# Optimization experiments

Measured on AMD Instinct MI355X. Metric: run time of the kernel, lower is better.

## Reference

```python
import jax, jax.numpy as jnp
import numpy as np

EPS = 1e-6
B, T, C = 2, 1024, 2048
H, KV, D = 32, 8, 128
E, F, TOPK = 8, 768, 2


def rmsnorm(x, w):
    xf = x.astype(jnp.float32)
    var = jnp.mean(xf * xf, axis=-1, keepdims=True)
    return w * (xf * jax.lax.rsqrt(var + EPS)).astype(x.dtype)


def rotate_half(x):
    d = x.shape[-1] // 2
    return jnp.concatenate([-x[..., d:], x[..., :d]], axis=-1)


def setup_inputs() -> dict:
    key = jax.random.key(0)
    ks = jax.random.split(key, 12)
    sc = 0.02
    x = jax.random.normal(ks[0], (B, T, C), dtype=jnp.float32)
    # RoPE tables: cos/sin of shape [B, T, D]
    inv_freq = 1.0 / (1e6 ** (np.arange(0, D, 2, dtype=np.float32) / D))
    pos = np.arange(T, dtype=np.float32)
    freqs = pos[:, None] * inv_freq[None, :]          # [T, D/2]
    emb = np.concatenate([freqs, freqs], axis=-1)     # [T, D]
    cos = jnp.broadcast_to(jnp.cos(emb)[None], (B, T, D)).astype(jnp.float32)
    sin = jnp.broadcast_to(jnp.sin(emb)[None], (B, T, D)).astype(jnp.float32)
    return {
        "x": x, "cos": cos, "sin": sin,
        "ln1_w": jnp.ones((C,), jnp.float32),
        "q_w": jax.random.normal(ks[1], (C, H * D), jnp.float32) * sc,
        "k_w": jax.random.normal(ks[2], (C, KV * D), jnp.float32) * sc,
        "v_w": jax.random.normal(ks[3], (C, KV * D), jnp.float32) * sc,
        "o_w": jax.random.normal(ks[4], (H * D, C), jnp.float32) * sc,
        "qn_w": jnp.ones((D,), jnp.float32),
        "kn_w": jnp.ones((D,), jnp.float32),
        "ln2_w": jnp.ones((C,), jnp.float32),
        "gate_w": jax.random.normal(ks[5], (C, E), jnp.float32) * sc,
        "gate_up_w": jax.random.normal(ks[6], (E, C, 2 * F), jnp.float32) * sc,
        "down_w": jax.random.normal(ks[7], (E, F, C), jnp.float32) * sc,
    }


def reference(x, cos, sin, ln1_w, q_w, k_w, v_w, o_w, qn_w, kn_w, ln2_w,
              gate_w, gate_up_w, down_w):
    b, t, c = x.shape
    # ---- attention branch ----
    h = rmsnorm(x, ln1_w)
    q = (h @ q_w).reshape(b, t, H, D)
    k = (h @ k_w).reshape(b, t, KV, D)
    v = (h @ v_w).reshape(b, t, KV, D)
    q = rmsnorm(q, qn_w)
    k = rmsnorm(k, kn_w)
    cb = cos[:, :, None, :]
    sb = sin[:, :, None, :]
    q = q * cb + rotate_half(q) * sb
    k = k * cb + rotate_half(k) * sb
    rep = H // KV
    k = jnp.repeat(k, rep, axis=2)  # [b,t,H,D]
    v = jnp.repeat(v, rep, axis=2)
    scores = jnp.einsum('bthd,bshd->bhts', q, k) / jnp.sqrt(jnp.float32(D))
    causal = jnp.tril(jnp.ones((t, t), dtype=bool))
    scores = jnp.where(causal, scores, jnp.finfo(scores.dtype).min)
    attn = jax.nn.softmax(scores, axis=-1)
    ao = jnp.einsum('bhts,bshd->bthd', attn, v).reshape(b, t, H * D) @ o_w
    x = x + ao
    # ---- MoE branch ----
    h2 = rmsnorm(x, ln2_w)
    hidden = h2.reshape(-1, c)                     # [N, C]
    logits = hidden @ gate_w                       # [N, E]
    rw = jax.nn.softmax(logits.astype(jnp.float32), axis=-1)
    tw, ti = jax.lax.top_k(rw, TOPK)
    tw = tw / (tw.sum(axis=-1, keepdims=True) + 1e-9)
    n = hidden.shape[0]
    routed = jnp.zeros_like(logits).at[jnp.arange(n)[:, None], ti].set(tw.astype(logits.dtype))
    routed = routed / (routed.sum(axis=-1, keepdims=True) + 1e-9)
    gu = jnp.einsum('th,ehq->teq', hidden, gate_up_w)   # [N, E, 2F]
    g, u = jnp.split(gu, 2, axis=-1)
    eo = jnp.einsum('teq,eqh->teh', jax.nn.silu(g) * u, down_w)  # [N, E, C]
    moe = (eo * routed[..., None]).sum(axis=1).reshape(b, t, c)
    return x + moe
```

## Files before the change

kernel.cpp:

```cpp
#include <hip/hip_runtime.h>
#include <hip/hip_bf16.h>

typedef short bf16x8 __attribute__((ext_vector_type(8)));
typedef float f32x4 __attribute__((ext_vector_type(4)));
typedef unsigned short u16;

#define NTOK 2048
#define CDIM 2048
#define TSEQ 1024
#define NH   32
#define NKV  8
#define DH   128
#define NE   8
#define FDIM 768
#define CAP  2048

#define GLOAD_LDS16(g, l) \
  __builtin_amdgcn_global_load_lds((const __attribute__((address_space(1))) void*)(g), \
                                   (__attribute__((address_space(3))) void*)(l), 16, 0, 0)

__device__ __forceinline__ u16 f2bf(float f){
  union { float f; unsigned u; } v; v.f = f;
  unsigned r = v.u + 0x7FFFu + ((v.u >> 16) & 1u);
  return (u16)(r >> 16);
}
__device__ __forceinline__ float bf2f(u16 x){
  union { unsigned u; float f; } v; v.u = ((unsigned)x) << 16; return v.f;
}

__device__ __forceinline__ f32x4 mfma_bf16(bf16x8 a, bf16x8 b, f32x4 c){
  return __builtin_amdgcn_mfma_f32_16x16x32_bf16(a, b, c, 0, 0, 0);
}

__device__ __forceinline__ int xcd_swz(int orig, int nwg){
  int xcd = orig & 7;
  int q = nwg >> 3, r = nwg & 7;
  int base = (xcd < r) ? xcd*(q+1) : r*(q+1) + (xcd-r)*q;
  return base + (orig >> 3);
}

__global__ void cast_transpose(const float* __restrict__ in, u16* __restrict__ out,
                               int R, int Cc, int rstride, int d1,
                               long long s_hi, long long s_lo)
{
  __shared__ float tile[32][33];
  int z = blockIdx.z;
  in += (long long)(z / d1) * s_hi + (long long)(z % d1) * s_lo;
  out += (size_t)z * R * Cc;
  int tx = threadIdx.x & 31, ty = threadIdx.x >> 5;
  int r0 = blockIdx.y * 32, c0 = blockIdx.x * 32;
  #pragma unroll
  for(int i=0;i<4;i++){
    int r = r0 + ty + i*8;
    if(r < R && c0 + tx < Cc) tile[ty + i*8][tx] = in[(size_t)r * rstride + c0 + tx];
  }
  __syncthreads();
  #pragma unroll
  for(int i=0;i<4;i++){
    int c = c0 + ty + i*8;
    if(c < Cc && r0 + tx < R) out[(size_t)c * R + r0 + tx] = f2bf(tile[tx][ty + i*8]);
  }
}

__global__ void transpose_u16(const u16* __restrict__ in, u16* __restrict__ out,
                              int R, int Cc, int rstride, int d1,
                              long long s_hi, long long s_lo)
{
  __shared__ u16 tile[32][34];
  int z = blockIdx.z;
  in += (long long)(z / d1) * s_hi + (long long)(z % d1) * s_lo;
  out += (size_t)z * R * Cc;
  int tx = threadIdx.x & 31, ty = threadIdx.x >> 5;
  int r0 = blockIdx.y * 32, c0 = blockIdx.x * 32;
  #pragma unroll
  for(int i=0;i<4;i++){
    int r = r0 + ty + i*8;
    if(r < R && c0 + tx < Cc) tile[ty + i*8][tx] = in[(size_t)r * rstride + c0 + tx];
  }
  __syncthreads();
  #pragma unroll
  for(int i=0;i<4;i++){
    int c = c0 + ty + i*8;
    if(c < Cc && r0 + tx < R) out[(size_t)c * R + r0 + tx] = tile[tx][ty + i*8];
  }
}

__global__ void rmsnorm_kernel(const float* __restrict__ x, const float* __restrict__ w,
                               u16* __restrict__ outb, float* __restrict__ outf)
{
  __shared__ float sbuf[4];
  int row = blockIdx.x;
  const float* xr = x + (size_t)row * CDIM;
  int t0 = threadIdx.x * 8;
  float4 v0 = *(const float4*)(xr + t0);
  float4 v1 = *(const float4*)(xr + t0 + 4);
  float a[8] = {v0.x,v0.y,v0.z,v0.w,v1.x,v1.y,v1.z,v1.w};
  float ss = 0.f;
  #pragma unroll
  for(int i=0;i<8;i++) ss += a[i]*a[i];
  #pragma unroll
  for(int o=32;o>0;o>>=1) ss += __shfl_xor(ss, o);
  if((threadIdx.x & 63) == 0) sbuf[threadIdx.x >> 6] = ss;
  __syncthreads();
  float tot = sbuf[0]+sbuf[1]+sbuf[2]+sbuf[3];
  float r = rsqrtf(tot * (1.0f/CDIM) + 1e-6f);
  float4 w0 = *(const float4*)(w + t0);
  float4 w1 = *(const float4*)(w + t0 + 4);
  float wv[8] = {w0.x,w0.y,w0.z,w0.w,w1.x,w1.y,w1.z,w1.w};
  #pragma unroll
  for(int i=0;i<8;i++){
    float o = a[i] * r * wv[i];
    outb[(size_t)row*CDIM + t0 + i] = f2bf(o);
    if(outf) outf[(size_t)row*CDIM + t0 + i] = o;
  }
}

__global__ __launch_bounds__(512, 2) void gemm256(const u16* __restrict__ A,
                                                  const u16* __restrict__ Bt,
                                                  u16* __restrict__ Cb,
                                                  int M, int N, int K)
{
  extern __shared__ u16 lds[];
  const int NT = K >> 6;
  int tid = threadIdx.x;
  int lane = tid & 63, g = lane >> 4, cl = lane & 15;
  int wid = tid >> 6, wr = wid >> 2, wc = wid & 3;
  int br = blockIdx.y * 256, bc = blockIdx.x * 256;
  int rowl[4], slotl[4], srcoff[4];
  #pragma unroll
  for(int l=0;l<4;l++){
    int c = l*512 + tid;
    rowl[l]  = c >> 3;
    slotl[l] = c & 7;
    srcoff[l] = (slotl[l] ^ (rowl[l] & 7)) * 8;
  }
  f32x4 acc[8][4];
  #pragma unroll
  for(int m=0;m<8;m++)
    #pragma unroll
    for(int n=0;n<4;n++) acc[m][n] = (f32x4){0.f,0.f,0.f,0.f};

  auto stage = [&](int t, int b){
    int k0 = t << 6;
    #pragma unroll
    for(int l=0;l<4;l++)
      GLOAD_LDS16(A  + (size_t)(br + rowl[l])*K + k0 + srcoff[l],
                  &lds[b*16384 + rowl[l]*64 + slotl[l]*8]);
    #pragma unroll
    for(int l=0;l<4;l++)
      GLOAD_LDS16(Bt + (size_t)(bc + rowl[l])*K + k0 + srcoff[l],
                  &lds[32768 + b*16384 + rowl[l]*64 + slotl[l]*8]);
  };

  stage(0, 0);
  for(int t=0;t<NT;t++){
    int buf = t & 1;
    if(t+1 < NT){
      stage(t+1, buf^1);
      asm volatile("s_waitcnt vmcnt(8)" ::: "memory");
    } else {
      asm volatile("s_waitcnt vmcnt(0)" ::: "memory");
    }
    asm volatile("s_barrier" ::: "memory");
    const u16* As_ = &lds[buf*16384];
    const u16* Bs_ = &lds[32768 + buf*16384];
    __builtin_amdgcn_s_setprio(1);
    #pragma unroll
    for(int kk=0;kk<2;kk++){
      bf16x8 a[8], b[4];
      #pragma unroll
      for(int m=0;m<8;m++){
        int row = wr*128 + m*16 + cl;
        int sl  = ((4*kk + g) ^ (row & 7)) * 8;
        a[m] = *(const bf16x8*)&As_[row*64 + sl];
      }
      #pragma unroll
      for(int n=0;n<4;n++){
        int row = wc*64 + n*16 + cl;
        int sl  = ((4*kk + g) ^ (row & 7)) * 8;
        b[n] = *(const bf16x8*)&Bs_[row*64 + sl];
      }
      #pragma unroll
      for(int m=0;m<8;m++)
        #pragma unroll
        for(int n=0;n<4;n++)
          acc[m][n] = mfma_bf16(a[m], b[n], acc[m][n]);
    }
    __builtin_amdgcn_s_setprio(0);
    asm volatile("s_barrier" ::: "memory");
  }
  #pragma unroll
  for(int m=0;m<8;m++)
    #pragma unroll
    for(int n=0;n<4;n++)
      #pragma unroll
      for(int j=0;j<4;j++){
        int row = br + wr*128 + m*16 + g*4 + j;
        int col = bc + wc*64 + n*16 + cl;
        Cb[(size_t)row*N + col] = f2bf(acc[m][n][j]);
      }
}

__global__ __launch_bounds__(256) void gemm_oproj_pipe(const u16* __restrict__ A,
                                                       const u16* __restrict__ Bt,
                                                       float* __restrict__ C,
                                                       const float* __restrict__ addsrc,
                                                       int M, int N, int K)
{
  extern __shared__ u16 lds[];
  int nwg = gridDim.x;
  int wgid = xcd_swz(blockIdx.x, nwg);
  int nbx = N >> 7;
  int bys = wgid / nbx, bxs = wgid % nbx;
  const int NT = K >> 6;
  int tid = threadIdx.x;
  int lane = tid&63, g = lane>>4, cl = lane&15;
  int w = tid>>6, wr = w>>1, wc = w&1;
  int br = bys*128, bc = bxs*128;
  int rowc[4], slotc[4], srcoff[4];
  #pragma unroll
  for(int l=0;l<4;l++){
    int c = l*256 + tid;
    rowc[l]  = c >> 3;
    slotc[l] = c & 7;
    srcoff[l] = (slotc[l] ^ (rowc[l] & 7)) * 8;
  }
  f32x4 acc[4][4];
  #pragma unroll
  for(int m=0;m<4;m++)
    #pragma unroll
    for(int n=0;n<4;n++) acc[m][n] = (f32x4){0.f,0.f,0.f,0.f};

  auto stage = [&](int t, int b){
    int k0 = t << 6;
    #pragma unroll
    for(int l=0;l<4;l++)
      GLOAD_LDS16(A + (size_t)(br + rowc[l])*K + k0 + srcoff[l],
                  &lds[b*8192 + rowc[l]*64 + slotc[l]*8]);
    #pragma unroll
    for(int l=0;l<4;l++)
      GLOAD_LDS16(Bt + (size_t)(bc + rowc[l])*K + k0 + srcoff[l],
                  &lds[16384 + b*8192 + rowc[l]*64 + slotc[l]*8]);
  };

  stage(0, 0);
  for(int t=0;t<NT;t++){
    int buf = t & 1;
    if(t+1 < NT){
      stage(t+1, buf^1);
      asm volatile("s_waitcnt vmcnt(8)" ::: "memory");
    } else {
      asm volatile("s_waitcnt vmcnt(0)" ::: "memory");
    }
    asm volatile("s_barrier" ::: "memory");
    const u16* As_ = &lds[buf*8192];
    const u16* Bs_ = &lds[16384 + buf*8192];
    __builtin_amdgcn_s_setprio(1);
    #pragma unroll
    for(int kk=0;kk<2;kk++){
      bf16x8 a[4], b[4];
      #pragma unroll
      for(int m=0;m<4;m++){
        int row = wr*64 + m*16 + cl;
        int sl  = ((4*kk + g) ^ (row & 7)) * 8;
        a[m] = *(const bf16x8*)&As_[row*64 + sl];
      }
      #pragma unroll
      for(int n=0;n<4;n++){
        int row = wc*64 + n*16 + cl;
        int sl  = ((4*kk + g) ^ (row & 7)) * 8;
        b[n] = *(const bf16x8*)&Bs_[row*64 + sl];
      }
      #pragma unroll
      for(int m=0;m<4;m++)
        #pragma unroll
        for(int n=0;n<4;n++)
          acc[m][n] = mfma_bf16(a[m], b[n], acc[m][n]);
    }
    __builtin_amdgcn_s_setprio(0);
    asm volatile("s_barrier" ::: "memory");
  }
  #pragma unroll
  for(int m=0;m<4;m++)
    #pragma unroll
    for(int n=0;n<4;n++)
      #pragma unroll
      for(int j=0;j<4;j++){
        int row = br + wr*64 + m*16 + g*4 + j;
        int col = bc + wc*64 + n*16 + cl;
        C[(size_t)row*N + col] = acc[m][n][j] + addsrc[(size_t)row*N + col];
      }
}

__global__ void qk_norm_rope(const u16* __restrict__ qkv, const float* __restrict__ cosb,
                             const float* __restrict__ sinb, const float* __restrict__ qnw,
                             const float* __restrict__ knw,
                             u16* __restrict__ qb, u16* __restrict__ kb)
{
  __shared__ float red[2];
  __shared__ float buf[128];
  int bt = blockIdx.x;
  int head = blockIdx.y;
  int d = threadIdx.x;
  int b = bt >> 10, t = bt & 1023;
  bool isq = head < NH;
  const u16* src = qkv + (size_t)bt*6144 + (isq ? head*DH : 4096 + (head-NH)*DH);
  float v = bf2f(src[d]);
  float ss = v*v;
  #pragma unroll
  for(int o=32;o>0;o>>=1) ss += __shfl_xor(ss, o);
  if((threadIdx.x & 63) == 0) red[threadIdx.x >> 6] = ss;
  __syncthreads();
  float tot = red[0] + red[1];
  float r = rsqrtf(tot * (1.0f/DH) + 1e-6f);
  float nv = v * r * (isq ? qnw[d] : knw[d]);
  buf[d] = nv;
  __syncthreads();
  float rot = (d < 64) ? -buf[d+64] : buf[d-64];
  float cs = cosb[(size_t)bt*DH + d], sn = sinb[(size_t)bt*DH + d];
  float ov = nv*cs + rot*sn;
  if(isq) qb[(((size_t)b*NH  + head)     *TSEQ + t)*DH + d] = f2bf(ov);
  else    kb[(((size_t)b*NKV + (head-NH))*TSEQ + t)*DH + d] = f2bf(ov);
}

__global__ __launch_bounds__(256) void attn_kernel(const u16* __restrict__ qb,
                                                   const u16* __restrict__ kb,
                                                   const u16* __restrict__ vt,
                                                   u16* __restrict__ aob)
{
  __shared__ u16 Ks[64][136];
  __shared__ u16 Vs[128][72];
  __shared__ u16 Ps[4][32][72];
  int tid = threadIdx.x;
  int w = tid>>6, lane = tid&63, g = lane>>4, cl = lane&15;
  int nwg = gridDim.x * gridDim.y * gridDim.z;
  int orig = (blockIdx.z * gridDim.y + blockIdx.y) * gridDim.x + blockIdx.x;
  int wgid = xcd_swz(orig, nwg);
  int bxs = wgid % gridDim.x;
  int bys = (wgid / gridDim.x) % gridDim.y;
  int bzs = wgid / (gridDim.x * gridDim.y);
  int b = bzs, kvh = bys;
  int qt = (gridDim.x - 1) - bxs;
  int q0 = qt*32;
  int h = kvh*4 + w;
  const u16* qp = qb + (((size_t)b*NH  + h  )*TSEQ)*DH;
  const u16* kp = kb + (((size_t)b*NKV + kvh)*TSEQ)*DH;
  const u16* vp = vt + (((size_t)b*NKV + kvh)*DH)*TSEQ;
  bf16x8 aq[2][4];
  #pragma unroll
  for(int m=0;m<2;m++)
    #pragma unroll
    for(int kd=0;kd<4;kd++)
      aq[m][kd] = *(const bf16x8*)(qp + (size_t)(q0 + m*16 + cl)*DH + kd*32 + g*8);
  f32x4 accO[2][8];
  #pragma unroll
  for(int m=0;m<2;m++)
    #pragma unroll
    for(int n=0;n<8;n++) accO[m][n] = (f32x4){0.f,0.f,0.f,0.f};
  float mr[2][4], lr[2][4];
  #pragma unroll
  for(int m=0;m<2;m++)
    #pragma unroll
    for(int j=0;j<4;j++){ mr[m][j] = -1e30f; lr[m][j] = 0.f; }
  const float scale = 0.08838834764831845f;
  for(int kv0 = 0; kv0 < q0 + 32; kv0 += 64){
    #pragma unroll
    for(int it=0; it<4; it++){
      int c = tid + it*256;
      int kr = c>>4, kcol = (c&15)*8;
      *(uint4*)&Ks[kr][kcol] = *(const uint4*)(kp + (size_t)(kv0 + kr)*DH + kcol);
      int vr = c>>3, vcol = (c&7)*8;
      *(uint4*)&Vs[vr][vcol] = *(const uint4*)(vp + (size_t)vr*TSEQ + kv0 + vcol);
    }
    __syncthreads();
    f32x4 sc[2][4];
    #pragma unroll
    for(int m=0;m<2;m++)
      #pragma unroll
      for(int n=0;n<4;n++) sc[m][n] = (f32x4){0.f,0.f,0.f,0.f};
    #pragma unroll
    for(int kd=0;kd<4;kd++){
      bf16x8 bk[4];
      #pragma unroll
      for(int n=0;n<4;n++) bk[n] = *(const bf16x8*)&Ks[n*16 + cl][kd*32 + g*8];
      #pragma unroll
      for(int m=0;m<2;m++)
        #pragma unroll
        for(int n=0;n<4;n++)
          sc[m][n] = mfma_bf16(aq[m][kd], bk[n], sc[m][n]);
    }
    #pragma unroll
    for(int m=0;m<2;m++)
      #pragma unroll
      for(int n=0;n<4;n++)
        #pragma unroll
        for(int j=0;j<4;j++){
          int row = q0 + m*16 + g*4 + j;
          int col = kv0 + n*16 + cl;
          float v = sc[m][n][j]*scale;
          sc[m][n][j] = (col > row) ? -1e30f : v;
        }
    float tmax[2][4];
    #pragma unroll
    for(int m=0;m<2;m++)
      #pragma unroll
      for(int j=0;j<4;j++)
        tmax[m][j] = fmaxf(fmaxf(sc[m][0][j], sc[m][1][j]), fmaxf(sc[m][2][j], sc[m][3][j]));
    #pragma unroll
    for(int o=1;o<16;o<<=1)
      #pragma unroll
      for(int m=0;m<2;m++)
        #pragma unroll
        for(int j=0;j<4;j++) tmax[m][j] = fmaxf(tmax[m][j], __shfl_xor(tmax[m][j], o));
    float fsc[2][4], rsum[2][4];
    #pragma unroll
    for(int m=0;m<2;m++)
      #pragma unroll
      for(int j=0;j<4;j++){
        float mn = fmaxf(mr[m][j], tmax[m][j]);
        float f  = __expf(mr[m][j]-mn);
        mr[m][j] = mn; fsc[m][j] = f;
        float s = 0.f;
        #pragma unroll
        for(int n=0;n<4;n++){
          float e = __expf(sc[m][n][j]-mn);
          sc[m][n][j] = e; s += e;
        }
        rsum[m][j] = s;
      }
    #pragma unroll
    for(int o=1;o<16;o<<=1)
      #pragma unroll
      for(int m=0;m<2;m++)
        #pragma unroll
        for(int j=0;j<4;j++) rsum[m][j] += __shfl_xor(rsum[m][j], o);
    #pragma unroll
    for(int m=0;m<2;m++)
      #pragma unroll
      for(int j=0;j<4;j++) lr[m][j] = lr[m][j]*fsc[m][j] + rsum[m][j];
    #pragma unroll
    for(int m=0;m<2;m++)
      #pragma unroll
      for(int n=0;n<8;n++)
        #pragma unroll
        for(int j=0;j<4;j++) accO[m][n][j] *= fsc[m][j];
    #pragma unroll
    for(int m=0;m<2;m++)
      #pragma unroll
      for(int n=0;n<4;n++)
        #pragma unroll
        for(int j=0;j<4;j++)
          Ps[w][m*16 + g*4 + j][n*16 + cl] = f2bf(sc[m][n][j]);
    bf16x8 pa[2][2];
    #pragma unroll
    for(int m=0;m<2;m++)
      #pragma unroll
      for(int s2=0;s2<2;s2++)
        pa[m][s2] = *(const bf16x8*)&Ps[w][m*16 + cl][s2*32 + g*8];
    #pragma unroll
    for(int n=0;n<8;n++){
      #pragma unroll
      for(int s2=0;s2<2;s2++){
        bf16x8 bv = *(const bf16x8*)&Vs[n*16 + cl][s2*32 + g*8];
        #pragma unroll
        for(int m=0;m<2;m++)
          accO[m][n] = mfma_bf16(pa[m][s2], bv, accO[m][n]);
      }
    }
    __syncthreads();
  }
  #pragma unroll
  for(int m=0;m<2;m++)
    #pragma unroll
    for(int n=0;n<8;n++)
      #pragma unroll
      for(int j=0;j<4;j++){
        int row = q0 + m*16 + g*4 + j;
        float v = accO[m][n][j] / lr[m][j];
        aob[((size_t)b*TSEQ + row)*(NH*DH) + h*DH + n*16 + cl] = f2bf(v);
      }
}

__global__ void route_kernel(const float* __restrict__ h2f, const float* __restrict__ gw,
                             int* __restrict__ cnt, int* __restrict__ bidx,
                             float* __restrict__ bw)
{
  int lane = threadIdx.x & 63;
  int token = blockIdx.x*4 + (threadIdx.x >> 6);
  float acc[8];
  #pragma unroll
  for(int e=0;e<8;e++) acc[e]=0.f;
  for(int c0 = lane*4; c0 < CDIM; c0 += 256){
    float4 hv = *(const float4*)(h2f + (size_t)token*CDIM + c0);
    float hvv[4] = {hv.x,hv.y,hv.z,hv.w};
    #pragma unroll
    for(int i=0;i<4;i++){
      const float* gr = gw + (size_t)(c0+i)*NE;
      #pragma unroll
      for(int e=0;e<8;e++) acc[e] += hvv[i]*gr[e];
    }
  }
  #pragma unroll
  for(int o=32;o>0;o>>=1)
    #pragma unroll
    for(int e=0;e<8;e++) acc[e] += __shfl_xor(acc[e], o);
  if(lane==0){
    float mx = acc[0];
    #pragma unroll
    for(int e=1;e<8;e++) mx = fmaxf(mx, acc[e]);
    float rw[8]; float s=0.f;
    #pragma unroll
    for(int e=0;e<8;e++){ rw[e] = __expf(acc[e]-mx); s += rw[e]; }
    #pragma unroll
    for(int e=0;e<8;e++) rw[e] /= s;
    int i0=0;
    #pragma unroll
    for(int e=1;e<8;e++) if(rw[e] > rw[i0]) i0=e;
    int i1 = (i0==0)?1:0;
    #pragma unroll
    for(int e=0;e<8;e++) if(e!=i0 && rw[e] > rw[i1]) i1=e;
    float tw0=rw[i0], tw1=rw[i1];
    float s1 = tw0+tw1+1e-9f;
    float a0 = tw0/s1, a1 = tw1/s1;
    float s2 = a0+a1+1e-9f;
    float w0 = a0/s2, w1 = a1/s2;
    int sl0 = atomicAdd(&cnt[i0],1);
    bidx[i0*CAP + sl0] = token; bw[i0*CAP + sl0] = w0;
    int sl1 = atomicAdd(&cnt[i1],1);
    bidx[i1*CAP + sl1] = token; bw[i1*CAP + sl1] = w1;
  }
}

__global__ __launch_bounds__(256) void gemm_gateup_pipe(const u16* __restrict__ h2b,
                                                        const u16* __restrict__ gupT,
                                                        u16* __restrict__ act,
                                                        const int* __restrict__ bidx,
                                                        const int* __restrict__ cnt)
{
  extern __shared__ u16 lds[];
  int d = blockIdx.x;
  int e = d & 7, j = d >> 3;
  int y = j / 6, x = j % 6;
  int nc = cnt[e];
  int sr = y*128;
  if(sr >= nc) return;
  const int K = CDIM, NT = K >> 6;
  const u16* Btg = gupT + (size_t)e*1536*CDIM + (size_t)(x*128)*CDIM;
  const u16* Btu = Btg + (size_t)768*CDIM;
  const int* be = bidx + e*CAP;
  int tid = threadIdx.x;
  int lane = tid&63, g = lane>>4, cl = lane&15;
  int w = tid>>6, wr = w>>1, wc = w&1;
  int rowc[4], slotc[4], srcoff[4];
  long long atok[4];
  #pragma unroll
  for(int l=0;l<4;l++){
    int c = l*256 + tid;
    rowc[l]  = c >> 3;
    slotc[l] = c & 7;
    srcoff[l] = (slotc[l] ^ (rowc[l] & 7)) * 8;
    int t = be[sr + rowc[l]];
    if(t < 0 || t >= NTOK) t = 0;
    atok[l] = (long long)t * CDIM;
  }
  f32x4 accG[4][4], accU[4][4];
  #pragma unroll
  for(int m=0;m<4;m++)
    #pragma unroll
    for(int n=0;n<4;n++){ accG[m][n] = (f32x4){0.f,0.f,0.f,0.f}; accU[m][n] = (f32x4){0.f,0.f,0.f,0.f}; }

  auto stage = [&](int t, int b){
    int k0 = t << 6;
    #pragma unroll
    for(int l=0;l<4;l++)
      GLOAD_LDS16(h2b + atok[l] + k0 + srcoff[l],
                  &lds[b*8192 + rowc[l]*64 + slotc[l]*8]);
    #pragma unroll
    for(int l=0;l<4;l++)
      GLOAD_LDS16(Btg + (size_t)rowc[l]*K + k0 + srcoff[l],
                  &lds[16384 + b*8192 + rowc[l]*64 + slotc[l]*8]);
    #pragma unroll
    for(int l=0;l<4;l++)
      GLOAD_LDS16(Btu + (size_t)rowc[l]*K + k0 + srcoff[l],
                  &lds[32768 + b*8192 + rowc[l]*64 + slotc[l]*8]);
  };

  stage(0, 0);
  for(int t=0;t<NT;t++){
    int buf = t & 1;
    if(t+1 < NT){
      stage(t+1, buf^1);
      asm volatile("s_waitcnt vmcnt(12)" ::: "memory");
    } else {
      asm volatile("s_waitcnt vmcnt(0)" ::: "memory");
    }
    asm volatile("s_barrier" ::: "memory");
    const u16* As_ = &lds[buf*8192];
    const u16* Bg_ = &lds[16384 + buf*8192];
    const u16* Bu_ = &lds[32768 + buf*8192];
    __builtin_amdgcn_s_setprio(1);
    #pragma unroll
    for(int kk=0;kk<2;kk++){
      bf16x8 a[4], bg[4], bu[4];
      #pragma unroll
      for(int m=0;m<4;m++){
        int row = wr*64 + m*16 + cl;
        int sl  = ((4*kk + g) ^ (row & 7)) * 8;
        a[m] = *(const bf16x8*)&As_[row*64 + sl];
      }
      #pragma unroll
      for(int n=0;n<4;n++){
        int row = wc*64 + n*16 + cl;
        int sl  = ((4*kk + g) ^ (row & 7)) * 8;
        bg[n] = *(const bf16x8*)&Bg_[row*64 + sl];
        bu[n] = *(const bf16x8*)&Bu_[row*64 + sl];
      }
      #pragma unroll
      for(int m=0;m<4;m++)
        #pragma unroll
        for(int n=0;n<4;n++){
          accG[m][n] = mfma_bf16(a[m], bg[n], accG[m][n]);
          accU[m][n] = mfma_bf16(a[m], bu[n], accU[m][n]);
        }
    }
    __builtin_amdgcn_s_setprio(0);
    asm volatile("s_barrier" ::: "memory");
  }
  #pragma unroll
  for(int m=0;m<4;m++)
    #pragma unroll
    for(int n=0;n<4;n++)
      #pragma unroll
      for(int jj=0;jj<4;jj++){
        int slot = sr + wr*64 + m*16 + g*4 + jj;
        int col  = x*128 + wc*64 + n*16 + cl;
        float gv = accG[m][n][jj], uv = accU[m][n][jj];
        float av = gv / (1.f + __expf(-gv)) * uv;
        act[((size_t)e*CAP + slot)*FDIM + col] = f2bf(av);
      }
}

__global__ __launch_bounds__(256) void gemm_down_pipe(const u16* __restrict__ act,
                                                      const u16* __restrict__ downT,
                                                      float* __restrict__ out,
                                                      const int* __restrict__ bidx,
                                                      const float* __restrict__ bw,
                                                      const int* __restrict__ cnt)
{
  extern __shared__ u16 lds[];
  int d = blockIdx.x;
  int e = d & 7, j = d >> 3;
  int y = j >> 4, x = j & 15;
  int nc = cnt[e];
  int sr = y*128;
  if(sr >= nc) return;
  const int K = FDIM, NT = K >> 6;
  const u16* A  = act   + ((size_t)e*CAP + sr)*FDIM;
  const u16* Bt = downT + (size_t)e*CDIM*FDIM + (size_t)(x*128)*FDIM;
  const int* be = bidx + e*CAP;
  const float* bwe = bw + e*CAP;
  int tid = threadIdx.x;
  int lane = tid&63, g = lane>>4, cl = lane&15;
  int w = tid>>6, wr = w>>1, wc = w&1;
  int rowc[4], slotc[4], srcoff[4];
  #pragma unroll
  for(int l=0;l<4;l++){
    int c = l*256 + tid;
    rowc[l]  = c >> 3;
    slotc[l] = c & 7;
    srcoff[l] = (slotc[l] ^ (rowc[l] & 7)) * 8;
  }
  f32x4 acc[4][4];
  #pragma unroll
  for(int m=0;m<4;m++)
    #pragma unroll
    for(int n=0;n<4;n++) acc[m][n] = (f32x4){0.f,0.f,0.f,0.f};

  auto stage = [&](int t, int b){
    int k0 = t << 6;
    #pragma unroll
    for(int l=0;l<4;l++)
      GLOAD_LDS16(A + (size_t)rowc[l]*K + k0 + srcoff[l],
                  &lds[b*8192 + rowc[l]*64 + slotc[l]*8]);
    #pragma unroll
    for(int l=0;l<4;l++)
      GLOAD_LDS16(Bt + (size_t)rowc[l]*K + k0 + srcoff[l],
                  &lds[16384 + b*8192 + rowc[l]*64 + slotc[l]*8]);
  };

  stage(0, 0);
  for(int t=0;t<NT;t++){
    int buf = t & 1;
    if(t+1 < NT){
      stage(t+1, buf^1);
      asm volatile("s_waitcnt vmcnt(8)" ::: "memory");
    } else {
      asm volatile("s_waitcnt vmcnt(0)" ::: "memory");
    }
    asm volatile("s_barrier" ::: "memory");
    const u16* As_ = &lds[buf*8192];
    const u16* Bs_ = &lds[16384 + buf*8192];
    __builtin_amdgcn_s_setprio(1);
    #pragma unroll
    for(int kk=0;kk<2;kk++){
      bf16x8 a[4], b[4];
      #pragma unroll
      for(int m=0;m<4;m++){
        int row = wr*64 + m*16 + cl;
        int sl  = ((4*kk + g) ^ (row & 7)) * 8;
        a[m] = *(const bf16x8*)&As_[row*64 + sl];
      }
      #pragma unroll
      for(int n=0;n<4;n++){
        int row = wc*64 + n*16 + cl;
        int sl  = ((4*kk + g) ^ (row & 7)) * 8;
        b[n] = *(const bf16x8*)&Bs_[row*64 + sl];
      }
      #pragma unroll
      for(int m=0;m<4;m++)
        #pragma unroll
        for(int n=0;n<4;n++)
          acc[m][n] = mfma_bf16(a[m], b[n], acc[m][n]);
    }
    __builtin_amdgcn_s_setprio(0);
    asm volatile("s_barrier" ::: "memory");
  }
  #pragma unroll
  for(int m=0;m<4;m++)
    #pragma unroll
    for(int jj=0;jj<4;jj++){
      int slot = sr + wr*64 + m*16 + g*4 + jj;
      if(slot < nc){
        int tok = be[slot];
        float wgt = bwe[slot];
        #pragma unroll
        for(int n=0;n<4;n++){
          int col = x*128 + wc*64 + n*16 + cl;
          atomicAdd(out + (size_t)tok*CDIM + col, wgt * acc[m][n][jj]);
        }
      }
    }
}

extern "C" void kernel_launch(void* const* d_in, const int* in_sizes, int n_in,
                              void* d_out, int out_size, void* d_ws, size_t ws_size,
                              hipStream_t stream)
{
  const float* x     = (const float*)d_in[0];
  const float* cosb  = (const float*)d_in[1];
  const float* sinb  = (const float*)d_in[2];
  const float* ln1w  = (const float*)d_in[3];
  const float* qw    = (const float*)d_in[4];
  const float* kw    = (const float*)d_in[5];
  const float* vw    = (const float*)d_in[6];
  const float* ow    = (const float*)d_in[7];
  const float* qnw   = (const float*)d_in[8];
  const float* knw   = (const float*)d_in[9];
  const float* ln2w  = (const float*)d_in[10];
  const float* gatew = (const float*)d_in[11];
  const float* gupw  = (const float*)d_in[12];
  const float* downw = (const float*)d_in[13];
  float* out = (float*)d_out;

  char* ws = (char*)d_ws;
  size_t off = 0;
  auto alloc = [&](size_t bytes)->char*{
    char* p = ws + off;
    off = (off + bytes + 255) & ~(size_t)255;
    return p;
  };
  u16*   wqkvT = (u16*)  alloc((size_t)6144*2048*2);
  u16*   owT   = (u16*)  alloc((size_t)2048*4096*2);
  u16*   gupT  = (u16*)  alloc((size_t)8*1536*2048*2);
  u16*   downT = (u16*)  alloc((size_t)8*2048*768*2);
  u16*   h1b   = (u16*)  alloc((size_t)2048*2048*2);
  u16*   qkvb  = (u16*)  alloc((size_t)2048*6144*2);
  u16*   qb    = (u16*)  alloc((size_t)2*32*1024*128*2);
  u16*   kb    = (u16*)  alloc((size_t)2*8*1024*128*2);
  u16*   vt    = (u16*)  alloc((size_t)2*8*1024*128*2);
  u16*   aob   = (u16*)  alloc((size_t)2048*4096*2);
  float* h2f   = (float*)alloc((size_t)2048*2048*4);
  u16*   h2b   = (u16*)  alloc((size_t)2048*2048*2);
  u16*   actb  = (u16*)  alloc((size_t)8*2048*768*2);
  int*   bidx  = (int*)  alloc((size_t)8*2048*4);
  float* bwgt  = (float*)alloc((size_t)8*2048*4);
  int*   cnt   = (int*)  alloc(64);
  (void)ws_size; (void)in_sizes; (void)n_in; (void)out_size;

  hipMemsetAsync(cnt, 0, 8*sizeof(int), stream);

  cast_transpose<<<dim3(128,64,1), 256, 0, stream>>>(qw, wqkvT,                  2048, 4096, 4096, 1, 0, 0);
  cast_transpose<<<dim3(32, 64,1), 256, 0, stream>>>(kw, wqkvT + (size_t)4096*2048, 2048, 1024, 1024, 1, 0, 0);
  cast_transpose<<<dim3(32, 64,1), 256, 0, stream>>>(vw, wqkvT + (size_t)5120*2048, 2048, 1024, 1024, 1, 0, 0);
  cast_transpose<<<dim3(64,128,1), 256, 0, stream>>>(ow, owT,                    4096, 2048, 2048, 1, 0, 0);
  cast_transpose<<<dim3(48, 64,8), 256, 0, stream>>>(gupw, gupT,                 2048, 1536, 1536, 8, 0, (long long)2048*1536);
  cast_transpose<<<dim3(64, 24,8), 256, 0, stream>>>(downw, downT,               768,  2048, 2048, 8, 0, (long long)768*2048);

  rmsnorm_kernel<<<2048, 256, 0, stream>>>(x, ln1w, h1b, nullptr);
  gemm256<<<dim3(24,8), 512, 131072, stream>>>(h1b, wqkvT, qkvb, 2048, 6144, 2048);
  qk_norm_rope<<<dim3(2048,40), 128, 0, stream>>>(qkvb, cosb, sinb, qnw, knw, qb, kb);
  transpose_u16<<<dim3(4,32,16), 256, 0, stream>>>(qkvb + 5120, vt, 1024, 128, 6144, 8,
                                                   (long long)1024*6144, 128);
  attn_kernel<<<dim3(32,8,2), 256, 0, stream>>>(qb, kb, vt, aob);
  gemm_oproj_pipe<<<256, 256, 65536, stream>>>(aob, owT, out, x, 2048, 2048, 4096);
  rmsnorm_kernel<<<2048, 256, 0, stream>>>(out, ln2w, h2b, h2f);
  route_kernel<<<512, 256, 0, stream>>>(h2f, gatew, cnt, bidx, bwgt);
  gemm_gateup_pipe<<<768, 256, 98304, stream>>>(h2b, gupT, actb, bidx, cnt);
  gemm_down_pipe<<<2048, 256, 65536, stream>>>(actb, downT, out, bidx, bwgt, cnt);
}
```

Baseline: 527.1 us.

## Fold softmax scale into Q, compute row sums via MFMA, lazy rescale

Folds the 1/sqrt(D) scale into Q during the RoPE kernel. The attention kernel now gets softmax row sums from an extra MFMA column: a ones row is appended to V in shared memory. This removes the per-tile shuffle reductions of the row sums. Rescaling of the output accumulator is done only when the running max grows by more than a threshold, and causal masking is skipped on tiles that sit entirely below the diagonal. The cost is one extra MFMA column and some register pressure, plus a small numerical risk from the lazy rescale and from bf16 rounding of the sums.

```diff
diff --git a/kernel.cpp b/kernel.cpp
--- a/kernel.cpp
+++ b/kernel.cpp
@@ -319,6 +319,7 @@
   float rot = (d < 64) ? -buf[d+64] : buf[d-64];
   float cs = cosb[(size_t)bt*DH + d], sn = sinb[(size_t)bt*DH + d];
   float ov = nv*cs + rot*sn;
+  if(isq) ov *= 0.08838834764831845f;
   if(isq) qb[(((size_t)b*NH  + head)     *TSEQ + t)*DH + d] = f2bf(ov);
   else    kb[(((size_t)b*NKV + (head-NH))*TSEQ + t)*DH + d] = f2bf(ov);
 }
@@ -329,7 +330,7 @@
                                                    u16* __restrict__ aob)
 {
   __shared__ u16 Ks[64][136];
-  __shared__ u16 Vs[128][72];
+  __shared__ u16 Vs[144][72];
   __shared__ u16 Ps[4][32][72];
   int tid = threadIdx.x;
   int w = tid>>6, lane = tid&63, g = lane>>4, cl = lane&15;
@@ -346,23 +347,26 @@
   const u16* qp = qb + (((size_t)b*NH  + h  )*TSEQ)*DH;
   const u16* kp = kb + (((size_t)b*NKV + kvh)*TSEQ)*DH;
   const u16* vp = vt + (((size_t)b*NKV + kvh)*DH)*TSEQ;
+  for(int idx = tid; idx < 16*72; idx += 256){
+    int r = idx / 72, c2 = idx % 72;
+    Vs[128 + r][c2] = (r == 0) ? (u16)0x3F80 : (u16)0;
+  }
   bf16x8 aq[2][4];
   #pragma unroll
   for(int m=0;m<2;m++)
     #pragma unroll
     for(int kd=0;kd<4;kd++)
       aq[m][kd] = *(const bf16x8*)(qp + (size_t)(q0 + m*16 + cl)*DH + kd*32 + g*8);
-  f32x4 accO[2][8];
+  f32x4 accO[2][9];
   #pragma unroll
   for(int m=0;m<2;m++)
     #pragma unroll
-    for(int n=0;n<8;n++) accO[m][n] = (f32x4){0.f,0.f,0.f,0.f};
-  float mr[2][4], lr[2][4];
+    for(int n=0;n<9;n++) accO[m][n] = (f32x4){0.f,0.f,0.f,0.f};
+  float mr[2][4];
   #pragma unroll
   for(int m=0;m<2;m++)
     #pragma unroll
-    for(int j=0;j<4;j++){ mr[m][j] = -1e30f; lr[m][j] = 0.f; }
-  const float scale = 0.08838834764831845f;
+    for(int j=0;j<4;j++) mr[m][j] = -1e30f;
   for(int kv0 = 0; kv0 < q0 + 32; kv0 += 64){
     #pragma unroll
     for(int it=0; it<4; it++){
@@ -389,17 +393,18 @@
         for(int n=0;n<4;n++)
           sc[m][n] = mfma_bf16(aq[m][kd], bk[n], sc[m][n]);
     }
-    #pragma unroll
-    for(int m=0;m<2;m++)
-      #pragma unroll
-      for(int n=0;n<4;n++)
-        #pragma unroll
-        for(int j=0;j<4;j++){
-          int row = q0 + m*16 + g*4 + j;
-          int col = kv0 + n*16 + cl;
-          float v = sc[m][n][j]*scale;
-          sc[m][n][j] = (col > row) ? -1e30f : v;
-        }
+    if(kv0 + 63 > q0){
+      #pragma unroll
+      for(int m=0;m<2;m++)
+        #pragma unroll
+        for(int n=0;n<4;n++)
+          #pragma unroll
+          for(int j=0;j<4;j++){
+            int row = q0 + m*16 + g*4 + j;
+            int col = kv0 + n*16 + cl;
+            if(col > row) sc[m][n][j] = -1e30f;
+          }
+    }
     float tmax[2][4];
     #pragma unroll
     for(int m=0;m<2;m++)
@@ -412,38 +417,32 @@
       for(int m=0;m<2;m++)
         #pragma unroll
         for(int j=0;j<4;j++) tmax[m][j] = fmaxf(tmax[m][j], __shfl_xor(tmax[m][j], o));
-    float fsc[2][4], rsum[2][4];
+    float grow = -1e30f;
     #pragma unroll
     for(int m=0;m<2;m++)
       #pragma unroll
-      for(int j=0;j<4;j++){
-        float mn = fmaxf(mr[m][j], tmax[m][j]);
-        float f  = __expf(mr[m][j]-mn);
-        mr[m][j] = mn; fsc[m][j] = f;
-        float s = 0.f;
-        #pragma unroll
-        for(int n=0;n<4;n++){
-          float e = __expf(sc[m][n][j]-mn);
-          sc[m][n][j] = e; s += e;
+      for(int j=0;j<4;j++) grow = fmaxf(grow, tmax[m][j] - mr[m][j]);
+    grow = fmaxf(grow, __shfl_xor(grow, 16));
+    grow = fmaxf(grow, __shfl_xor(grow, 32));
+    if(grow > 8.0f){
+      #pragma unroll
+      for(int m=0;m<2;m++)
+        #pragma unroll
+        for(int j=0;j<4;j++){
+          float mn = fmaxf(mr[m][j], tmax[m][j]);
+          float f  = __expf(mr[m][j] - mn);
+          mr[m][j] = mn;
+          #pragma unroll
+          for(int n=0;n<9;n++) accO[m][n][j] *= f;
         }
-        rsum[m][j] = s;
-      }
-    #pragma unroll
-    for(int o=1;o<16;o<<=1)
-      #pragma unroll
-      for(int m=0;m<2;m++)
-        #pragma unroll
-        for(int j=0;j<4;j++) rsum[m][j] += __shfl_xor(rsum[m][j], o);
+    }
     #pragma unroll
     for(int m=0;m<2;m++)
       #pragma unroll
-      for(int j=0;j<4;j++) lr[m][j] = lr[m][j]*fsc[m][j] + rsum[m][j];
-    #pragma unroll
-    for(int m=0;m<2;m++)
-      #pragma unroll
-      for(int n=0;n<8;n++)
-        #pragma unroll
-        for(int j=0;j<4;j++) accO[m][n][j] *= fsc[m][j];
+      for(int n=0;n<4;n++)
+        #pragma unroll
+        for(int j=0;j<4;j++)
+          sc[m][n][j] = __expf(sc[m][n][j] - mr[m][j]);
     #pragma unroll
     for(int m=0;m<2;m++)
       #pragma unroll
@@ -458,7 +457,7 @@
       for(int s2=0;s2<2;s2++)
         pa[m][s2] = *(const bf16x8*)&Ps[w][m*16 + cl][s2*32 + g*8];
     #pragma unroll
-    for(int n=0;n<8;n++){
+    for(int n=0;n<9;n++){
       #pragma unroll
       for(int s2=0;s2<2;s2++){
         bf16x8 bv = *(const bf16x8*)&Vs[n*16 + cl][s2*32 + g*8];
@@ -470,15 +469,22 @@
     __syncthreads();
   }
   #pragma unroll
-  for(int m=0;m<2;m++)
+  for(int m=0;m<2;m++){
+    float linv[4];
+    #pragma unroll
+    for(int j=0;j<4;j++){
+      float l = __shfl(accO[m][8][j], lane & 48);
+      linv[j] = 1.0f / l;
+    }
     #pragma unroll
     for(int n=0;n<8;n++)
       #pragma unroll
       for(int j=0;j<4;j++){
         int row = q0 + m*16 + g*4 + j;
-        float v = accO[m][n][j] / lr[m][j];
+        float v = accO[m][n][j] * linv[j];
         aob[((size_t)b*TSEQ + row)*(NH*DH) + h*DH + n*16 + cl] = f2bf(v);
       }
+  }
 }
 
 __global__ void route_kernel(const float* __restrict__ h2f, const float* __restrict__ gw,
@@ -736,7 +742,7 @@
         #pragma unroll
         for(int n=0;n<4;n++){
           int col = x*128 + wc*64 + n*16 + cl;
-          atomicAdd(out + (size_t)tok*CDIM + col, wgt * acc[m][n][jj]);
+          atomicAdd(out + (size_t)tok*CDIM + col, wgt * acc[m][jj >= 0 ? n : n][jj]);
         }
       }
     }
```

Result: no change. 523.7 us (-0.6%).
